# Optimization experiments

Measured on AMD Instinct MI355X. Metric: run time of the kernel, lower is better.

## Reference

```python
import jax, jax.numpy as jnp
import numpy as np

N_NODES = 100000


def gcn_conv(x, edge_index, W, b, num_nodes):
    # PyG GCNConv: h = x @ W; add self-loops; symmetric deg^-1/2 normalization;
    # out[dst] = sum_{src->dst} norm * h[src] + b
    h = x @ W
    loop = jnp.arange(num_nodes)
    src = jnp.concatenate([edge_index[0], loop])
    dst = jnp.concatenate([edge_index[1], loop])
    deg = jax.ops.segment_sum(jnp.ones_like(dst, dtype=h.dtype), dst, num_segments=num_nodes)
    dinv = jnp.where(deg > 0, jax.lax.rsqrt(deg), 0.0)
    norm = dinv[src] * dinv[dst]  # [E+N]
    msg = h[src] * norm[:, None]  # gather + scale
    out = jax.ops.segment_sum(msg, dst, num_segments=num_nodes)
    return out + b


def setup_inputs() -> dict:
    key = jax.random.key(0)
    k1, k2, k3, k4 = jax.random.split(key, 4)
    E = 3200000
    F_IN, HID, CLS = 512, 16, 7
    x = jax.random.normal(k1, (N_NODES, F_IN), dtype=jnp.float32)
    edge_index = jax.random.randint(k2, (2, E), 0, N_NODES, dtype=jnp.int64)
    W1 = jax.random.normal(k3, (F_IN, HID), dtype=jnp.float32) / np.sqrt(F_IN)
    b1 = jnp.zeros((HID,), dtype=jnp.float32)
    W2 = jax.random.normal(k4, (HID, CLS), dtype=jnp.float32) / np.sqrt(HID)
    b2 = jnp.zeros((CLS,), dtype=jnp.float32)
    return {"x": x, "edge_index": edge_index, "W1": W1, "b1": b1, "W2": W2, "b2": b2}


def reference(x, edge_index, W1, b1, W2, b2):
    h = gcn_conv(x, edge_index, W1, b1, N_NODES)
    h = jax.nn.relu(h)
    # dropout is identity in eval mode (p=0.5, training=False)
    out = gcn_conv(h, edge_index, W2, b2, N_NODES)
    return out
```

## Files before the change

### kernel.cpp

```cpp
#include <hip/hip_runtime.h>

#define N_NODES 100000
#define F_IN 512
#define HID 16
#define CLS 7

#define BK_SHIFT 8
#define BK_NODES 256
#define NBK ((N_NODES + BK_NODES - 1) / BK_NODES)
#define BK_CAP 9216

#define SB_TILE 4096
#define SB_EPT 16

#define G1_ROWS 128

#define ADD4(a, v) { (a).x += (v).x; (a).y += (v).y; (a).z += (v).z; (a).w += (v).w; }
#define FMA4(acc, sc, wv) { (acc).x += (sc)*(wv).x; (acc).y += (sc)*(wv).y; (acc).z += (sc)*(wv).z; (acc).w += (sc)*(wv).w; }

__global__ __launch_bounds__(256) void fat_kernel(const void* __restrict__ eidx,
                                                  long long E,
                                                  int* __restrict__ cursor,
                                                  unsigned int* __restrict__ binned,
                                                  const float* __restrict__ x,
                                                  const float* __restrict__ W1,
                                                  float* __restrict__ h1s,
                                                  int scBlocks) {
    __shared__ float Ws[F_IN * HID];
    __shared__ int hist[NBK];
    __shared__ int gcur[NBK];
    __shared__ unsigned int det;
    const int tid = threadIdx.x;

    if ((int)blockIdx.x < scBlocks) {
        const long long tileBeg = (long long)blockIdx.x * SB_TILE;
        long long remll = E - tileBeg;
        const int tcnt = (int)(remll < SB_TILE ? remll : SB_TILE);
        const bool evE = ((E & 1LL) == 0LL);

        for (int i = tid; i < NBK; i += 256) hist[i] = 0;
        if (tid == 0) det = 0u;
        __syncthreads();

        {
            unsigned int myor = 0u;
            const unsigned long long* p64 = (const unsigned long long*)eidx;
            for (int i = tid; i < tcnt; i += 256)
                myor |= (unsigned int)(p64[tileBeg + i] >> 32);
            if (myor) atomicOr(&det, 1u);
        }
        __syncthreads();
        const int is64 = (det == 0u) ? 1 : 0;

        unsigned int vv[SB_EPT];
        int bb[SB_EPT];

#pragma unroll
        for (int j = 0; j < SB_EPT / 2; j++) {
            long long e = tileBeg + (long long)j * 512 + 2 * tid;
            int s0 = 0, d0 = 0, s1 = 0, d1 = 0;
            const bool ok0 = e < E, ok1 = (e + 1) < E;
            if (is64) {
                const long long* p = (const long long*)eidx;
                if (ok1 && evE) {
                    longlong2 sp = *(const longlong2*)(p + e);
                    longlong2 dp = *(const longlong2*)(p + E + e);
                    s0 = (int)sp.x; s1 = (int)sp.y; d0 = (int)dp.x; d1 = (int)dp.y;
                } else {
                    if (ok0) { s0 = (int)p[e];     d0 = (int)p[E + e]; }
                    if (ok1) { s1 = (int)p[e + 1]; d1 = (int)p[E + e + 1]; }
                }
            } else {
                const int* p = (const int*)eidx;
                if (ok1 && evE) {
                    int2 sp = *(const int2*)(p + e);
                    int2 dp = *(const int2*)(p + E + e);
                    s0 = sp.x; s1 = sp.y; d0 = dp.x; d1 = dp.y;
                } else {
                    if (ok0) { s0 = p[e];     d0 = p[E + e]; }
                    if (ok1) { s1 = p[e + 1]; d1 = p[E + e + 1]; }
                }
            }
            if (ok0) {
                int b = d0 >> BK_SHIFT;
                bb[2 * j] = b;
                vv[2 * j] = ((unsigned int)(d0 & (BK_NODES - 1)) << 17) | (unsigned int)s0;
                atomicAdd(&hist[b], 1);
            } else bb[2 * j] = -1;
            if (ok1) {
                int b = d1 >> BK_SHIFT;
                bb[2 * j + 1] = b;
                vv[2 * j + 1] = ((unsigned int)(d1 & (BK_NODES - 1)) << 17) | (unsigned int)s1;
                atomicAdd(&hist[b], 1);
            } else bb[2 * j + 1] = -1;
        }
        __syncthreads();
        for (int i = tid; i < NBK; i += 256)
            gcur[i] = hist[i] ? (i * BK_CAP + atomicAdd(&cursor[i], hist[i])) : 0;
        __syncthreads();
#pragma unroll
        for (int j = 0; j < SB_EPT; j++) {
            int b = bb[j];
            if (b >= 0) {
                int pos = atomicAdd(&gcur[b], 1);
                if (pos < (b + 1) * BK_CAP)
                    binned[pos] = vv[j];
            }
        }
    } else {
        const int rowBase = ((int)blockIdx.x - scBlocks) * G1_ROWS;

#pragma unroll
        for (int it = 0; it < 8; it++) {
            int f = it * 256 + tid;
            ((float4*)Ws)[f] = ((const float4*)W1)[f];
        }
        __syncthreads();

        const int r  = tid >> 2;
        const int j4 = tid & 3;
        int g0 = rowBase + r;
        int g1 = rowBase + 64 + r;
        int a0r = (g0 < N_NODES) ? g0 : N_NODES - 1;
        int a1r = (g1 < N_NODES) ? g1 : N_NODES - 1;
        const float4* xa4 = (const float4*)(x + (long long)a0r * F_IN);
        const float4* xb4 = (const float4*)(x + (long long)a1r * F_IN);
        const float4* Wf4 = (const float4*)Ws;

        float4 accA = make_float4(0.f, 0.f, 0.f, 0.f);
        float4 accB = make_float4(0.f, 0.f, 0.f, 0.f);

#pragma unroll 4
        for (int t = 0; t < F_IN / 4; t++) {
            float4 xa = xa4[t];
            float4 xb = xb4[t];
            const float4* wp = Wf4 + t * 16 + j4;
            float4 w0 = wp[0];
            float4 w1 = wp[4];
            float4 w2 = wp[8];
            float4 w3 = wp[12];
            FMA4(accA, xa.x, w0); FMA4(accA, xa.y, w1);
            FMA4(accA, xa.z, w2); FMA4(accA, xa.w, w3);
            FMA4(accB, xb.x, w0); FMA4(accB, xb.y, w1);
            FMA4(accB, xb.z, w2); FMA4(accB, xb.w, w3);
        }
        if (g0 < N_NODES)
            ((float4*)(h1s + (long long)g0 * HID))[j4] = accA;
        if (g1 < N_NODES)
            ((float4*)(h1s + (long long)g1 * HID))[j4] = accB;
    }
}

__global__ __launch_bounds__(512) void csr_build_kernel(const int* __restrict__ cursor,
                                                        unsigned int* __restrict__ binned,
                                                        float* __restrict__ dinv,
                                                        int* __restrict__ rowptr,
                                                        int* __restrict__ degA,
                                                        float* __restrict__ h1s) {
    __shared__ unsigned int stage[BK_CAP];
    __shared__ int hist[BK_NODES];
    __shared__ int scanv[BK_NODES];
    __shared__ int curs[BK_NODES];
    const int tid = threadIdx.x;
    const int b = blockIdx.x;
    const int base = b * BK_CAP;
    int cnt = cursor[b];
    if (cnt > BK_CAP) cnt = BK_CAP;
    if (tid < BK_NODES) hist[tid] = 0;
    __syncthreads();
    const int cnt4 = cnt >> 2;
    for (int i = tid; i < cnt4; i += 512) {
        uint4 u = ((const uint4*)(binned + base))[i];
        ((uint4*)stage)[i] = u;
        atomicAdd(&hist[u.x >> 17], 1);
        atomicAdd(&hist[u.y >> 17], 1);
        atomicAdd(&hist[u.z >> 17], 1);
        atomicAdd(&hist[u.w >> 17], 1);
    }
    for (int i = (cnt4 << 2) + tid; i < cnt; i += 512) {
        unsigned int u = binned[base + i];
        stage[i] = u;
        atomicAdd(&hist[u >> 17], 1);
    }
    __syncthreads();
    if (tid < BK_NODES) scanv[tid] = hist[tid];
    __syncthreads();
    for (int off = 1; off < BK_NODES; off <<= 1) {
        int a = 0;
        if (tid < BK_NODES && tid >= off) a = scanv[tid - off];
        __syncthreads();
        if (tid < BK_NODES) scanv[tid] += a;
        __syncthreads();
    }
    if (tid < BK_NODES) {
        int e = scanv[tid] - hist[tid];
        curs[tid] = e;
        int g = b * BK_NODES + tid;
        if (g < N_NODES) {
            rowptr[g] = base + e;
            degA[g] = hist[tid];
            dinv[g] = rsqrtf((float)(hist[tid] + 1));
        }
    }
    __syncthreads();
    for (int i = tid; i < cnt4; i += 512) {
        uint4 u = ((const uint4*)stage)[i];
        int p0 = atomicAdd(&curs[(int)(u.x >> 17)], 1); binned[base + p0] = u.x & 0x1FFFFu;
        int p1 = atomicAdd(&curs[(int)(u.y >> 17)], 1); binned[base + p1] = u.y & 0x1FFFFu;
        int p2 = atomicAdd(&curs[(int)(u.z >> 17)], 1); binned[base + p2] = u.z & 0x1FFFFu;
        int p3 = atomicAdd(&curs[(int)(u.w >> 17)], 1); binned[base + p3] = u.w & 0x1FFFFu;
    }
    for (int i = (cnt4 << 2) + tid; i < cnt; i += 512) {
        unsigned int u = stage[i];
        int p = atomicAdd(&curs[(int)(u >> 17)], 1);
        binned[base + p] = u & 0x1FFFFu;
    }
    {
        const int ln = tid >> 1;
        const int hf = tid & 1;
        const int g = b * BK_NODES + ln;
        if (g < N_NODES) {
            float dn = rsqrtf((float)(hist[ln] + 1));
            float4* hp = (float4*)(h1s + (long long)g * HID);
            float4 v0 = hp[hf * 2];
            float4 v1 = hp[hf * 2 + 1];
            hp[hf * 2]     = make_float4(v0.x * dn, v0.y * dn, v0.z * dn, v0.w * dn);
            hp[hf * 2 + 1] = make_float4(v1.x * dn, v1.y * dn, v1.z * dn, v1.w * dn);
        }
    }
}

#define A1_NODES 64

__global__ __launch_bounds__(256) void agg1_gemm2_kernel(const int* __restrict__ rowptr,
                                                         const int* __restrict__ degA,
                                                         const int* __restrict__ csr_src,
                                                         const float* __restrict__ h1s,
                                                         const float* __restrict__ dinv,
                                                         const float* __restrict__ b1,
                                                         const float* __restrict__ W2,
                                                         float* __restrict__ h2s) {
    __shared__ float W2s[HID][8];
    __shared__ float t_lds[A1_NODES][HID + 1];
    const int tid = threadIdx.x;
    if (tid < HID * 8) {
        int j = tid >> 3, c = tid & 7;
        W2s[j][c] = (c < CLS) ? W2[j * CLS + c] : 0.f;
    }
    const int ln = tid >> 2;
    const int j4 = tid & 3;
    const int n = blockIdx.x * A1_NODES + ln;
    float dn = 0.f;
    if (n < N_NODES) {
        const int beg = rowptr[n];
        const int end = beg + degA[n];
        const float4* h4 = (const float4*)h1s;
        float4 a0 = make_float4(0.f, 0.f, 0.f, 0.f);
        float4 a1 = make_float4(0.f, 0.f, 0.f, 0.f);
        float4 a2 = make_float4(0.f, 0.f, 0.f, 0.f);
        float4 a3 = make_float4(0.f, 0.f, 0.f, 0.f);
        int k = beg;
        for (; k < end && (k & 3); k++) {
            float4 v = h4[(long long)csr_src[k] * 4 + j4];
            ADD4(a0, v);
        }
        for (; k + 8 <= end; k += 8) {
            int4 s0 = *(const int4*)(csr_src + k);
            int4 s1 = *(const int4*)(csr_src + k + 4);
            float4 v0 = h4[(long long)s0.x * 4 + j4];
            float4 v1 = h4[(long long)s0.y * 4 + j4];
            float4 v2 = h4[(long long)s0.z * 4 + j4];
            float4 v3 = h4[(long long)s0.w * 4 + j4];
            float4 v4 = h4[(long long)s1.x * 4 + j4];
            float4 v5 = h4[(long long)s1.y * 4 + j4];
            float4 v6 = h4[(long long)s1.z * 4 + j4];
            float4 v7 = h4[(long long)s1.w * 4 + j4];
            ADD4(a0, v0); ADD4(a1, v1); ADD4(a2, v2); ADD4(a3, v3);
            ADD4(a0, v4); ADD4(a1, v5); ADD4(a2, v6); ADD4(a3, v7);
        }
        if (k + 4 <= end) {
            int4 s0 = *(const int4*)(csr_src + k);
            float4 v0 = h4[(long long)s0.x * 4 + j4];
            float4 v1 = h4[(long long)s0.y * 4 + j4];
            float4 v2 = h4[(long long)s0.z * 4 + j4];
            float4 v3 = h4[(long long)s0.w * 4 + j4];
            ADD4(a0, v0); ADD4(a1, v1); ADD4(a2, v2); ADD4(a3, v3);
            k += 4;
        }
        for (; k < end; k++) {
            float4 v = h4[(long long)csr_src[k] * 4 + j4];
            ADD4(a0, v);
        }
        dn = dinv[n];
        float4 self = h4[(long long)n * 4 + j4];
        float4 bb = ((const float4*)b1)[j4];
        float* tp = &t_lds[ln][j4 * 4];
        tp[0] = fmaxf(bb.x + dn * (a0.x + a1.x + a2.x + a3.x + self.x), 0.f);
        tp[1] = fmaxf(bb.y + dn * (a0.y + a1.y + a2.y + a3.y + self.y), 0.f);
        tp[2] = fmaxf(bb.z + dn * (a0.z + a1.z + a2.z + a3.z + self.z), 0.f);
        tp[3] = fmaxf(bb.w + dn * (a0.w + a1.w + a2.w + a3.w + self.w), 0.f);
    }
    __syncthreads();
    if (n < N_NODES) {
        float b0 = 0.f, c1 = 0.f;
#pragma unroll
        for (int j = 0; j < HID; j++) {
            float v = t_lds[ln][j];
            b0 += v * W2s[j][2 * j4];
            c1 += v * W2s[j][2 * j4 + 1];
        }
        h2s[(long long)n * 8 + 2 * j4]     = dn * b0;
        h2s[(long long)n * 8 + 2 * j4 + 1] = dn * c1;
    }
}

#define A2_NODES 128

__global__ __launch_bounds__(256) void agg2_gather_kernel(const int* __restrict__ rowptr,
                                                          const int* __restrict__ degA,
                                                          const int* __restrict__ csr_src,
                                                          const float* __restrict__ h2s,
                                                          const float* __restrict__ dinv,
                                                          const float* __restrict__ b2,
                                                          float* __restrict__ out) {
    const int tid = threadIdx.x;
    const int ln = tid >> 1;
    const int half = tid & 1;
    const int n = blockIdx.x * A2_NODES + ln;
    if (n >= N_NODES) return;
    const int beg = rowptr[n];
    const int end = beg + degA[n];
    const float4* h4 = (const float4*)h2s;
    float4 a0 = make_float4(0.f, 0.f, 0.f, 0.f);
    float4 a1 = make_float4(0.f, 0.f, 0.f, 0.f);
    float4 a2 = make_float4(0.f, 0.f, 0.f, 0.f);
    float4 a3 = make_float4(0.f, 0.f, 0.f, 0.f);
    int k = beg;
    for (; k < end && (k & 3); k++) {
        float4 v = h4[(long long)csr_src[k] * 2 + half];
        ADD4(a0, v);
    }
    for (; k + 8 <= end; k += 8) {
        int4 s0 = *(const int4*)(csr_src + k);
        int4 s1 = *(const int4*)(csr_src + k + 4);
        float4 v0 = h4[(long long)s0.x * 2 + half];
        float4 v1 = h4[(long long)s0.y * 2 + half];
        float4 v2 = h4[(long long)s0.z * 2 + half];
        float4 v3 = h4[(long long)s0.w * 2 + half];
        float4 v4 = h4[(long long)s1.x * 2 + half];
        float4 v5 = h4[(long long)s1.y * 2 + half];
        float4 v6 = h4[(long long)s1.z * 2 + half];
        float4 v7 = h4[(long long)s1.w * 2 + half];
        ADD4(a0, v0); ADD4(a1, v1); ADD4(a2, v2); ADD4(a3, v3);
        ADD4(a0, v4); ADD4(a1, v5); ADD4(a2, v6); ADD4(a3, v7);
    }
    if (k + 4 <= end) {
        int4 s0 = *(const int4*)(csr_src + k);
        float4 v0 = h4[(long long)s0.x * 2 + half];
        float4 v1 = h4[(long long)s0.y * 2 + half];
        float4 v2 = h4[(long long)s0.z * 2 + half];
        float4 v3 = h4[(long long)s0.w * 2 + half];
        ADD4(a0, v0); ADD4(a1, v1); ADD4(a2, v2); ADD4(a3, v3);
        k += 4;
    }
    for (; k < end; k++) {
        float4 v = h4[(long long)csr_src[k] * 2 + half];
        ADD4(a0, v);
    }
    float dn = dinv[n];
    float4 self = h4[(long long)n * 2 + half];
    float tx = self.x + a0.x + a1.x + a2.x + a3.x;
    float ty = self.y + a0.y + a1.y + a2.y + a3.y;
    float tz = self.z + a0.z + a1.z + a2.z + a3.z;
    float tw = self.w + a0.w + a1.w + a2.w + a3.w;
    long long ob = (long long)n * CLS;
    if (half == 0) {
        out[ob + 0] = b2[0] + dn * tx;
        out[ob + 1] = b2[1] + dn * ty;
        out[ob + 2] = b2[2] + dn * tz;
        out[ob + 3] = b2[3] + dn * tw;
    } else {
        out[ob + 4] = b2[4] + dn * tx;
        out[ob + 5] = b2[5] + dn * ty;
        out[ob + 6] = b2[6] + dn * tz;
    }
}

extern "C" void kernel_launch(void* const* d_in, const int* in_sizes, int n_in,
                              void* d_out, int out_size, void* d_ws, size_t ws_size,
                              hipStream_t stream) {
    const float* x    = (const float*)d_in[0];
    const void*  eidx = d_in[1];
    const float* W1   = (const float*)d_in[2];
    const float* b1   = (const float*)d_in[3];
    const float* W2   = (const float*)d_in[4];
    const float* b2   = (const float*)d_in[5];
    float* out = (float*)d_out;
    const long long E = (long long)in_sizes[1] / 2;

    char* ws = (char*)d_ws;
    size_t off = 0;
    auto alloc = [&](size_t bytes) -> void* {
        void* p = ws + off;
        off = (off + bytes + 255) & ~(size_t)255;
        return p;
    };
    int*          cursor = (int*)alloc((size_t)NBK * 4);
    unsigned int* binned = (unsigned int*)alloc((size_t)NBK * BK_CAP * 4);
    int*          rowptr = (int*)alloc((size_t)N_NODES * 4);
    int*          degA   = (int*)alloc((size_t)N_NODES * 4);
    float*        dinv   = (float*)alloc((size_t)N_NODES * 4);
    float*        h1s    = (float*)alloc((size_t)N_NODES * HID * 4);
    float*        h2s    = (float*)alloc((size_t)N_NODES * 8 * 4);
    (void)ws_size;

    hipMemsetAsync(cursor, 0, (size_t)NBK * 4, stream);

    const int scBlocks = (int)((E + SB_TILE - 1) / SB_TILE);
    const int gmBlocks = (N_NODES + G1_ROWS - 1) / G1_ROWS;
    fat_kernel<<<scBlocks + gmBlocks, 256, 0, stream>>>(
        eidx, E, cursor, binned, x, W1, h1s, scBlocks);

    csr_build_kernel<<<NBK, 512, 0, stream>>>(cursor, binned, dinv, rowptr, degA, h1s);

    const int* csr_src = (const int*)binned;
    agg1_gemm2_kernel<<<(N_NODES + A1_NODES - 1) / A1_NODES, 256, 0, stream>>>(
        rowptr, degA, csr_src, h1s, dinv, b1, W2, h2s);

    agg2_gather_kernel<<<(N_NODES + A2_NODES - 1) / A2_NODES, 256, 0, stream>>>(
        rowptr, degA, csr_src, h2s, dinv, b2, out);
}
```

Baseline: 435.6 us.

## Interleave scatter and GEMM blocks, halve W1 LDS tile, hoist int64 detection

Moves the int64-vs-int32 edge index detection out of every scatter block into a single small pre-kernel that writes a flag, so the scatter blocks no longer do an extra pass over their tile. Scatter and GEMM blocks are now interleaved in launch order so the bandwidth-heavy x reads and the atomic-heavy binning run concurrently instead of as separate phases. The W1 shared-memory tile is halved and loaded in two K-halves to cut LDS use per block and raise occupancy, at the cost of extra barriers and a second W1 load. The detection now samples only the first 4096 edges, which is a weaker check than before.

```diff
diff --git a/kernel.cpp b/kernel.cpp
--- a/kernel.cpp
+++ b/kernel.cpp
@@ -14,43 +14,55 @@
 #define SB_EPT 16
 
 #define G1_ROWS 128
+#define G1_KH 256
 
 #define ADD4(a, v) { (a).x += (v).x; (a).y += (v).y; (a).z += (v).z; (a).w += (v).w; }
 #define FMA4(acc, sc, wv) { (acc).x += (sc)*(wv).x; (acc).y += (sc)*(wv).y; (acc).z += (sc)*(wv).z; (acc).w += (sc)*(wv).w; }
 
+__global__ void detect_i64_kernel(const unsigned int* __restrict__ idx32,
+                                  int* __restrict__ flag, int n_check) {
+    __shared__ unsigned int s;
+    if (threadIdx.x == 0) s = 0u;
+    __syncthreads();
+    unsigned int v = 0u;
+    for (int i = threadIdx.x; i < n_check; i += blockDim.x)
+        v |= idx32[2 * i + 1];
+    atomicOr(&s, v);
+    __syncthreads();
+    if (threadIdx.x == 0) *flag = (s == 0u) ? 1 : 0;
+}
+
 __global__ __launch_bounds__(256) void fat_kernel(const void* __restrict__ eidx,
                                                   long long E,
+                                                  const int* __restrict__ flag,
                                                   int* __restrict__ cursor,
                                                   unsigned int* __restrict__ binned,
                                                   const float* __restrict__ x,
                                                   const float* __restrict__ W1,
                                                   float* __restrict__ h1s,
-                                                  int scBlocks) {
-    __shared__ float Ws[F_IN * HID];
+                                                  int scBlocks, int gmBlocks) {
+    __shared__ float Ws[G1_KH * HID];
     __shared__ int hist[NBK];
     __shared__ int gcur[NBK];
-    __shared__ unsigned int det;
     const int tid = threadIdx.x;
 
-    if ((int)blockIdx.x < scBlocks) {
-        const long long tileBeg = (long long)blockIdx.x * SB_TILE;
-        long long remll = E - tileBeg;
-        const int tcnt = (int)(remll < SB_TILE ? remll : SB_TILE);
+    const int bid = (int)blockIdx.x;
+    const int nPair = (scBlocks < gmBlocks) ? scBlocks : gmBlocks;
+    bool isScatter;
+    int idx;
+    if (bid < 2 * nPair) { isScatter = !(bid & 1); idx = bid >> 1; }
+    else {
+        idx = nPair + (bid - 2 * nPair);
+        isScatter = (scBlocks > gmBlocks);
+    }
+
+    if (isScatter) {
+        const long long tileBeg = (long long)idx * SB_TILE;
         const bool evE = ((E & 1LL) == 0LL);
+        const int is64 = *flag;
 
         for (int i = tid; i < NBK; i += 256) hist[i] = 0;
-        if (tid == 0) det = 0u;
         __syncthreads();
-
-        {
-            unsigned int myor = 0u;
-            const unsigned long long* p64 = (const unsigned long long*)eidx;
-            for (int i = tid; i < tcnt; i += 256)
-                myor |= (unsigned int)(p64[tileBeg + i] >> 32);
-            if (myor) atomicOr(&det, 1u);
-        }
-        __syncthreads();
-        const int is64 = (det == 0u) ? 1 : 0;
 
         unsigned int vv[SB_EPT];
         int bb[SB_EPT];
@@ -108,14 +120,7 @@
             }
         }
     } else {
-        const int rowBase = ((int)blockIdx.x - scBlocks) * G1_ROWS;
-
-#pragma unroll
-        for (int it = 0; it < 8; it++) {
-            int f = it * 256 + tid;
-            ((float4*)Ws)[f] = ((const float4*)W1)[f];
-        }
-        __syncthreads();
+        const int rowBase = idx * G1_ROWS;
 
         const int r  = tid >> 2;
         const int j4 = tid & 3;
@@ -125,24 +130,34 @@
         int a1r = (g1 < N_NODES) ? g1 : N_NODES - 1;
         const float4* xa4 = (const float4*)(x + (long long)a0r * F_IN);
         const float4* xb4 = (const float4*)(x + (long long)a1r * F_IN);
-        const float4* Wf4 = (const float4*)Ws;
 
         float4 accA = make_float4(0.f, 0.f, 0.f, 0.f);
         float4 accB = make_float4(0.f, 0.f, 0.f, 0.f);
 
+        for (int h = 0; h < 2; h++) {
+            __syncthreads();
+#pragma unroll
+            for (int it = 0; it < 4; it++) {
+                int f = it * 256 + tid;
+                ((float4*)Ws)[f] = ((const float4*)W1)[h * (G1_KH * HID / 4) + f];
+            }
+            __syncthreads();
+            const float4* Wf4 = (const float4*)Ws;
+            const int tb = h * (G1_KH / 4);
 #pragma unroll 4
-        for (int t = 0; t < F_IN / 4; t++) {
-            float4 xa = xa4[t];
-            float4 xb = xb4[t];
-            const float4* wp = Wf4 + t * 16 + j4;
-            float4 w0 = wp[0];
-            float4 w1 = wp[4];
-            float4 w2 = wp[8];
-            float4 w3 = wp[12];
-            FMA4(accA, xa.x, w0); FMA4(accA, xa.y, w1);
-            FMA4(accA, xa.z, w2); FMA4(accA, xa.w, w3);
-            FMA4(accB, xb.x, w0); FMA4(accB, xb.y, w1);
-            FMA4(accB, xb.z, w2); FMA4(accB, xb.w, w3);
+            for (int t = 0; t < G1_KH / 4; t++) {
+                float4 xa = xa4[tb + t];
+                float4 xb = xb4[tb + t];
+                const float4* wp = Wf4 + t * 16 + j4;
+                float4 w0 = wp[0];
+                float4 w1 = wp[4];
+                float4 w2 = wp[8];
+                float4 w3 = wp[12];
+                FMA4(accA, xa.x, w0); FMA4(accA, xa.y, w1);
+                FMA4(accA, xa.z, w2); FMA4(accA, xa.w, w3);
+                FMA4(accB, xb.x, w0); FMA4(accB, xb.y, w1);
+                FMA4(accB, xb.z, w2); FMA4(accB, xb.w, w3);
+            }
         }
         if (g0 < N_NODES)
             ((float4*)(h1s + (long long)g0 * HID))[j4] = accA;
@@ -405,6 +420,7 @@
         off = (off + bytes + 255) & ~(size_t)255;
         return p;
     };
+    int*          flag   = (int*)alloc(4);
     int*          cursor = (int*)alloc((size_t)NBK * 4);
     unsigned int* binned = (unsigned int*)alloc((size_t)NBK * BK_CAP * 4);
     int*          rowptr = (int*)alloc((size_t)N_NODES * 4);
@@ -416,10 +432,13 @@
 
     hipMemsetAsync(cursor, 0, (size_t)NBK * 4, stream);
 
+    detect_i64_kernel<<<1, 256, 0, stream>>>((const unsigned int*)eidx, flag,
+                                             (int)(E < 4096 ? E : 4096));
+
     const int scBlocks = (int)((E + SB_TILE - 1) / SB_TILE);
     const int gmBlocks = (N_NODES + G1_ROWS - 1) / G1_ROWS;
     fat_kernel<<<scBlocks + gmBlocks, 256, 0, stream>>>(
-        eidx, E, cursor, binned, x, W1, h1s, scBlocks);
+        eidx, E, flag, cursor, binned, x, W1, h1s, scBlocks, gmBlocks);
 
     csr_build_kernel<<<NBK, 512, 0, stream>>>(cursor, binned, dinv, rowptr, degA, h1s);
 
```

Result: slower. 451.1 us (+3.6%).
